# Performance work log

Hardware: AMD Instinct MI355X
Metric: run time of the kernel (lower is better)

The kernel has to match this reference:

```python
import jax, jax.numpy as jnp
import numpy as np

N, E, H, C, L, D, OUT = 50000, 800000, 4, 32, 3, 128, 64
EPS = 1e-5


def setup_inputs() -> dict:
    key = jax.random.key(0)
    ks = jax.random.split(key, 16)
    s = 1.0 / np.sqrt(D)
    return {
        "x": jax.random.normal(ks[0], (N, D), jnp.float32),
        "edge_index": jax.random.randint(ks[1], (2, E), 0, N, dtype=jnp.int32),
        "Wq": jax.random.normal(ks[2], (L, D, H * C), jnp.float32) * s,
        "bq": jax.random.normal(ks[3], (L, H * C), jnp.float32) * 0.02,
        "Wk": jax.random.normal(ks[4], (L, D, H * C), jnp.float32) * s,
        "bk": jax.random.normal(ks[5], (L, H * C), jnp.float32) * 0.02,
        "Wv": jax.random.normal(ks[6], (L, D, H * C), jnp.float32) * s,
        "bv": jax.random.normal(ks[7], (L, H * C), jnp.float32) * 0.02,
        "Ws": jax.random.normal(ks[8], (L, D, H * C), jnp.float32) * s,
        "bs": jax.random.normal(ks[9], (L, H * C), jnp.float32) * 0.02,
        "bn_g": jnp.ones((L, H * C), jnp.float32),
        "bn_b": jnp.zeros((L, H * C), jnp.float32),
        "W_out": jax.random.normal(ks[10], (D, OUT), jnp.float32) * s,
        "b_out": jax.random.normal(ks[11], (OUT,), jnp.float32) * 0.02,
        "bno_g": jnp.ones((OUT,), jnp.float32),
        "bno_b": jnp.zeros((OUT,), jnp.float32),
    }


def _batch_norm(x, g, b):
    # training-mode BatchNorm1d: per-feature batch mean/var (biased), eps=1e-5
    mu = x.mean(axis=0)
    var = x.var(axis=0)
    return g * (x - mu) * jax.lax.rsqrt(var + EPS) + b


def _transformer_conv(x, src, dst, Wq, bq, Wk, bk, Wv, bv, Ws, bs):
    n = x.shape[0]
    q = (x @ Wq + bq).reshape(n, H, C)  # query at target nodes
    k = (x @ Wk + bk).reshape(n, H, C)
    v = (x @ Wv + bv).reshape(n, H, C)
    # per-edge attention logits [E, H]
    score = (q[dst] * k[src]).sum(-1) / jnp.sqrt(jnp.float32(C))
    # numerically-stable softmax over incoming edges of each target node
    m = jax.ops.segment_max(score, dst, num_segments=n)
    ex = jnp.exp(score - m[dst])
    denom = jax.ops.segment_sum(ex, dst, num_segments=n)
    alpha = ex / denom[dst]  # [E, H]
    agg = jax.ops.segment_sum(v[src] * alpha[..., None], dst, num_segments=n)
    out = agg.reshape(n, H * C) + x @ Ws + bs  # concat heads + root/skip term
    return out


def reference(x, edge_index, Wq, bq, Wk, bk, Wv, bv, Ws, bs, bn_g, bn_b,
              W_out, b_out, bno_g, bno_b):
    src, dst = edge_index[0], edge_index[1]
    h = x
    for i in range(L):
        h = _transformer_conv(h, src, dst, Wq[i], bq[i], Wk[i], bk[i],
                              Wv[i], bv[i], Ws[i], bs[i])
        h = _batch_norm(h, bn_g[i], bn_b[i])
        h = jax.nn.relu(h)
    h = h @ W_out + b_out
    h = _batch_norm(h, bno_g, bno_b)
    return jax.nn.relu(h)
```

## Files before the change

### kernel.cpp

```cpp
#include <hip/hip_runtime.h>
#include <hip/hip_bf16.h>
#include <math.h>

#define D_FEAT 128
#define NLAYER 3
#define BN_EPS 1e-5f
#define INV_SQRT_C 0.17677669529663687f
#define SORT_NPB 1024
#define NREP 8

typedef __bf16 bf16x8 __attribute__((ext_vector_type(8)));
typedef float f32x4 __attribute__((ext_vector_type(4)));

static __device__ __forceinline__ unsigned short f2bf(float f) {
    return __builtin_bit_cast(unsigned short, __float2bfloat16(f));
}
static __device__ __forceinline__ float bfl(unsigned u) { return __uint_as_float(u << 16); }
static __device__ __forceinline__ float bfh(unsigned u) { return __uint_as_float(u & 0xffff0000u); }
static __device__ __forceinline__ unsigned packbf(float a, float b) {
    return (unsigned)f2bf(a) | ((unsigned)f2bf(b) << 16);
}


__global__ void cvt_bf16_kernel(const float* __restrict__ src, unsigned short* __restrict__ dst,
                                size_t n4) {
    for (size_t t = (size_t)blockIdx.x * blockDim.x + threadIdx.x; t < n4;
         t += (size_t)gridDim.x * blockDim.x) {
        size_t i = t * 4;
        float4 v = *(const float4*)(src + i);
        ushort4 u;
        u.x = f2bf(v.x); u.y = f2bf(v.y); u.z = f2bf(v.z); u.w = f2bf(v.w);
        *(ushort4*)(dst + i) = u;
    }
}

__global__ void prep_weights_kernel(
    const float* __restrict__ Wq, const float* __restrict__ Wk,
    const float* __restrict__ Wv, const float* __restrict__ Ws,
    const float* __restrict__ Wo,
    unsigned short* __restrict__ Wt, unsigned short* __restrict__ Wot)
{
    const int permat = 16384;
    const int main_total = NLAYER * 4 * permat;
    const int total = main_total + 64 * 128;
    for (int i = blockIdx.x * blockDim.x + threadIdx.x; i < total;
         i += gridDim.x * blockDim.x) {
        if (i < main_total) {
            int l = i / (4 * permat);
            int rem = i - l * (4 * permat);
            int mat = rem / permat;
            int e = rem - mat * permat;
            int nn = e >> 7;
            int kk = e & 127;
            const float* src = (mat == 0) ? Wq : (mat == 1) ? Wk : (mat == 2) ? Wv : Ws;
            Wt[(size_t)l * 4 * permat + mat * permat + nn * 128 + kk] =
                f2bf(src[(size_t)l * permat + kk * 128 + nn]);
        } else {
            int e = i - main_total;
            int nn = e >> 7;
            int kk = e & 127;
            Wot[nn * 128 + kk] = f2bf(Wo[kk * 64 + nn]);
        }
    }
}


__global__ void hist_kernel(const int* __restrict__ dst, int E, int* __restrict__ deg) {
    int e = blockIdx.x * blockDim.x + threadIdx.x;
    if (e < E) atomicAdd(&deg[dst[e]], 1);
}

__global__ __launch_bounds__(256) void scan1_kernel(const int* __restrict__ deg, int n,
                                                    int* __restrict__ rowptr,
                                                    int* __restrict__ partials) {
    int b = blockIdx.x, tid = threadIdx.x;
    int base = b * 1024 + tid * 4;
    int4 d = {0, 0, 0, 0};
    if (base + 3 < n) d = *(const int4*)(deg + base);
    else {
        if (base + 0 < n) d.x = deg[base + 0];
        if (base + 1 < n) d.y = deg[base + 1];
        if (base + 2 < n) d.z = deg[base + 2];
        if (base + 3 < n) d.w = deg[base + 3];
    }
    int p0 = d.x, p1 = p0 + d.y, p2 = p1 + d.z, p3 = p2 + d.w;
    int v = p3;
    int lane = tid & 63;
    #pragma unroll
    for (int off = 1; off < 64; off <<= 1) {
        int t = __shfl_up(v, off);
        if (lane >= off) v += t;
    }
    __shared__ int wsum[4];
    int w = tid >> 6;
    if (lane == 63) wsum[w] = v;
    __syncthreads();
    int woff = 0;
    #pragma unroll
    for (int j = 0; j < 4; ++j) if (j < w) woff += wsum[j];
    int excl = woff + v - p3;
    if (base + 0 < n) rowptr[base + 1] = excl + p0;
    if (base + 1 < n) rowptr[base + 2] = excl + p1;
    if (base + 2 < n) rowptr[base + 3] = excl + p2;
    if (base + 3 < n) rowptr[base + 4] = excl + p3;
    if (tid == 255) partials[b] = excl + p3;
    if (b == 0 && tid == 0) rowptr[0] = 0;
}

__global__ void scan2_kernel(int* __restrict__ partials, int nb) {
    int lane = threadIdx.x;
    int v = (lane < nb) ? partials[lane] : 0;
    #pragma unroll
    for (int off = 1; off < 64; off <<= 1) {
        int t = __shfl_up(v, off);
        if (lane >= off) v += t;
    }
    if (lane < nb) partials[lane] = v;
}

__global__ __launch_bounds__(256) void scan3_kernel(int* __restrict__ rowptr, int n,
                                                    const int* __restrict__ partials) {
    int b = blockIdx.x, tid = threadIdx.x;
    if (b == 0) return;
    int off = partials[b - 1];
    int base = b * 1024 + tid * 4;
    #pragma unroll
    for (int j = 0; j < 4; ++j) {
        int i = base + j;
        if (i < n) rowptr[i + 1] += off;
    }
}

__global__ void scatter_kernel(const int* __restrict__ src, const int* __restrict__ dst, int E,
                               const int* __restrict__ rowptr, int* __restrict__ cursor,
                               int* __restrict__ csrsrc) {
    int e = blockIdx.x * blockDim.x + threadIdx.x;
    if (e < E) {
        int d = dst[e];
        int p = atomicAdd(&cursor[d], 1);
        csrsrc[rowptr[d] + p] = src[e];
    }
}


__global__ __launch_bounds__(256) void bin_blockhist_kernel(
    const int* __restrict__ rowptr, int n, int B, int* __restrict__ bhist)
{
    __shared__ int h[256];
    int b = blockIdx.x, tid = threadIdx.x;
    h[tid] = 0;
    __syncthreads();
    #pragma unroll
    for (int j = 0; j < SORT_NPB / 256; ++j) {
        int i = b * SORT_NPB + j * 256 + tid;
        if (i < n) {
            int d = rowptr[i + 1] - rowptr[i];
            if (d > 255) d = 255;
            atomicAdd(&h[255 - d], 1);
        }
    }
    __syncthreads();
    bhist[tid * B + b] = h[tid];
}

__global__ __launch_bounds__(256) void bin_colscan_kernel(
    int* __restrict__ bhist, int B, int* __restrict__ binoff)
{
    int d = threadIdx.x;
    int run = 0;
    for (int b = 0; b < B; ++b) {
        int c = bhist[d * B + b];
        bhist[d * B + b] = run;
        run += c;
    }
    __shared__ int sd[256];
    sd[d] = run;
    __syncthreads();
    int v = run;
    for (int s = 1; s < 256; s <<= 1) {
        int t = (d >= s) ? sd[d - s] : 0;
        __syncthreads();
        sd[d] += t;
        __syncthreads();
    }
    binoff[d] = sd[d] - v;
}

__global__ __launch_bounds__(256) void bin_order_kernel(
    const int* __restrict__ rowptr, int n, int B,
    const int* __restrict__ bhist, const int* __restrict__ binoff,
    int* __restrict__ order)
{
    __shared__ int cur[256];
    int b = blockIdx.x, tid = threadIdx.x;
    cur[tid] = binoff[tid] + bhist[tid * B + b];
    __syncthreads();
    #pragma unroll
    for (int j = 0; j < SORT_NPB / 256; ++j) {
        int i = b * SORT_NPB + j * 256 + tid;
        if (i < n) {
            int d = rowptr[i + 1] - rowptr[i];
            if (d > 255) d = 255;
            int pos = atomicAdd(&cur[255 - d], 1);
            order[pos] = i;
        }
    }
}


__global__ __launch_bounds__(256, 2) void gemm_qkvs_kernel(
    const unsigned short* __restrict__ A,
    const float* __restrict__ stats, const float* __restrict__ g,
    const float* __restrict__ bb, int mode, int M,
    const unsigned short* __restrict__ Wt,
    const float* __restrict__ b0, const float* __restrict__ b1,
    const float* __restrict__ b2, const float* __restrict__ b3,
    unsigned short* __restrict__ q, unsigned short* __restrict__ kv,
    unsigned short* __restrict__ s)
{
    __shared__ float scale[128], shift[128];
    int r0 = blockIdx.x * 128;
    int tid = threadIdx.x;
    int wid = tid >> 6, lane = tid & 63;
    int wm = wid >> 1, wn = wid & 1;
    int lr = lane & 15, lk = lane >> 4;

    if (mode && tid < 128) {
        float ssum = 0.f, qsum = 0.f;
        #pragma unroll
        for (int r = 0; r < NREP; ++r) {
            ssum += stats[r * 1024 + tid];
            qsum += stats[r * 1024 + 512 + tid];
        }
        float invN = 1.0f / (float)M;
        float mu = ssum * invN;
        float var = qsum * invN - mu * mu;
        float sc = rsqrtf(var + BN_EPS) * g[tid];
        scale[tid] = sc;
        shift[tid] = bb[tid] - mu * sc;
    }
    __syncthreads();

    bf16x8 a[4][4];
    #pragma unroll
    for (int ks = 0; ks < 4; ++ks) {
        int ko = ks * 32 + lk * 8;
        #pragma unroll
        for (int mi = 0; mi < 4; ++mi) {
            int arow = r0 + wm * 64 + mi * 16 + lr;
            int4 t = {0, 0, 0, 0};
            if (arow < M) t = *(const int4*)(A + (size_t)arow * 128 + ko);
            if (mode) {
                float4 sc0 = *(const float4*)&scale[ko];
                float4 sc1 = *(const float4*)&scale[ko + 4];
                float4 sh0 = *(const float4*)&shift[ko];
                float4 sh1 = *(const float4*)&shift[ko + 4];
                float v0 = fmaxf(bfl(t.x) * sc0.x + sh0.x, 0.f);
                float v1 = fmaxf(bfh(t.x) * sc0.y + sh0.y, 0.f);
                float v2 = fmaxf(bfl(t.y) * sc0.z + sh0.z, 0.f);
                float v3 = fmaxf(bfh(t.y) * sc0.w + sh0.w, 0.f);
                float v4 = fmaxf(bfl(t.z) * sc1.x + sh1.x, 0.f);
                float v5 = fmaxf(bfh(t.z) * sc1.y + sh1.y, 0.f);
                float v6 = fmaxf(bfl(t.w) * sc1.z + sh1.z, 0.f);
                float v7 = fmaxf(bfh(t.w) * sc1.w + sh1.w, 0.f);
                t.x = (int)packbf(v0, v1); t.y = (int)packbf(v2, v3);
                t.z = (int)packbf(v4, v5); t.w = (int)packbf(v6, v7);
            }
            a[mi][ks] = __builtin_bit_cast(bf16x8, t);
        }
    }

    #pragma unroll
    for (int cc = 0; cc < 2; ++cc) {
        int ct = blockIdx.y * 2 + cc;
        const unsigned short* W = Wt + (size_t)ct * 16384;

        f32x4 acc[4][4] = {};
        #pragma unroll
        for (int ks = 0; ks < 4; ++ks) {
            int ko = ks * 32 + lk * 8;
            bf16x8 b[4];
            #pragma unroll
            for (int nj = 0; nj < 4; ++nj) {
                int4 t = *(const int4*)(W + (size_t)(wn * 64 + nj * 16 + lr) * 128 + ko);
                b[nj] = __builtin_bit_cast(bf16x8, t);
            }
            #pragma unroll
            for (int mi = 0; mi < 4; ++mi)
                #pragma unroll
                for (int nj = 0; nj < 4; ++nj)
                    acc[mi][nj] = __builtin_amdgcn_mfma_f32_16x16x32_bf16(
                        a[mi][ks], b[nj], acc[mi][nj], 0, 0, 0);
        }

        const float* bias = (ct == 0) ? b0 : (ct == 1) ? b1 : (ct == 2) ? b2 : b3;
        #pragma unroll
        for (int mi = 0; mi < 4; ++mi) {
            #pragma unroll
            for (int nj = 0; nj < 4; ++nj) {
                int col = wn * 64 + nj * 16 + lr;
                float bv = bias[col];
                #pragma unroll
                for (int reg = 0; reg < 4; ++reg) {
                    int rw = r0 + wm * 64 + mi * 16 + lk * 4 + reg;
                    if (rw < M) {
                        unsigned short val = f2bf(acc[mi][nj][reg] + bv);
                        if (ct == 0) q[(size_t)rw * 128 + col] = val;
                        else if (ct == 1) kv[(size_t)rw * 256 + col] = val;
                        else if (ct == 2) kv[(size_t)rw * 256 + 128 + col] = val;
                        else s[(size_t)rw * 128 + col] = val;
                    }
                }
            }
        }
    }
}

__global__ __launch_bounds__(256, 2) void gemm_final_kernel(
    const unsigned short* __restrict__ A,
    const float* __restrict__ stats, const float* __restrict__ g,
    const float* __restrict__ bb, int M,
    const unsigned short* __restrict__ Wot, const float* __restrict__ bias,
    float* __restrict__ out, float* __restrict__ statsOut)
{
    __shared__ float scale[128], shift[128];
    __shared__ float fs[64], fq[64];
    int r0 = blockIdx.x * 128;
    int tid = threadIdx.x;
    int wid = tid >> 6, lane = tid & 63;
    int wm = wid >> 1, wn = wid & 1;
    int lr = lane & 15, lk = lane >> 4;

    if (tid < 128) {
        float ssum = 0.f, qsum = 0.f;
        #pragma unroll
        for (int r = 0; r < NREP; ++r) {
            ssum += stats[r * 1024 + tid];
            qsum += stats[r * 1024 + 512 + tid];
        }
        float invN = 1.0f / (float)M;
        float mu = ssum * invN;
        float var = qsum * invN - mu * mu;
        float sc = rsqrtf(var + BN_EPS) * g[tid];
        scale[tid] = sc;
        shift[tid] = bb[tid] - mu * sc;
    }
    if (tid < 64) { fs[tid] = 0.f; fq[tid] = 0.f; }
    __syncthreads();

    bf16x8 a[4][4];
    #pragma unroll
    for (int ks = 0; ks < 4; ++ks) {
        int ko = ks * 32 + lk * 8;
        #pragma unroll
        for (int mi = 0; mi < 4; ++mi) {
            int arow = r0 + wm * 64 + mi * 16 + lr;
            int4 t = {0, 0, 0, 0};
            if (arow < M) t = *(const int4*)(A + (size_t)arow * 128 + ko);
            float4 sc0 = *(const float4*)&scale[ko];
            float4 sc1 = *(const float4*)&scale[ko + 4];
            float4 sh0 = *(const float4*)&shift[ko];
            float4 sh1 = *(const float4*)&shift[ko + 4];
            float v0 = fmaxf(bfl(t.x) * sc0.x + sh0.x, 0.f);
            float v1 = fmaxf(bfh(t.x) * sc0.y + sh0.y, 0.f);
            float v2 = fmaxf(bfl(t.y) * sc0.z + sh0.z, 0.f);
            float v3 = fmaxf(bfh(t.y) * sc0.w + sh0.w, 0.f);
            float v4 = fmaxf(bfl(t.z) * sc1.x + sh1.x, 0.f);
            float v5 = fmaxf(bfh(t.z) * sc1.y + sh1.y, 0.f);
            float v6 = fmaxf(bfl(t.w) * sc1.z + sh1.z, 0.f);
            float v7 = fmaxf(bfh(t.w) * sc1.w + sh1.w, 0.f);
            t.x = (int)packbf(v0, v1); t.y = (int)packbf(v2, v3);
            t.z = (int)packbf(v4, v5); t.w = (int)packbf(v6, v7);
            a[mi][ks] = __builtin_bit_cast(bf16x8, t);
        }
    }

    f32x4 acc[4][2] = {};
    #pragma unroll
    for (int ks = 0; ks < 4; ++ks) {
        int ko = ks * 32 + lk * 8;
        bf16x8 b[2];
        #pragma unroll
        for (int nj = 0; nj < 2; ++nj) {
            int4 t = *(const int4*)(Wot + (size_t)(wn * 32 + nj * 16 + lr) * 128 + ko);
            b[nj] = __builtin_bit_cast(bf16x8, t);
        }
        #pragma unroll
        for (int mi = 0; mi < 4; ++mi)
            #pragma unroll
            for (int nj = 0; nj < 2; ++nj)
                acc[mi][nj] = __builtin_amdgcn_mfma_f32_16x16x32_bf16(
                    a[mi][ks], b[nj], acc[mi][nj], 0, 0, 0);
    }

    float csum[2] = {0.f, 0.f}, csq[2] = {0.f, 0.f};
    #pragma unroll
    for (int mi = 0; mi < 4; ++mi) {
        #pragma unroll
        for (int nj = 0; nj < 2; ++nj) {
            int col = wn * 32 + nj * 16 + lr;
            float bv = bias[col];
            #pragma unroll
            for (int reg = 0; reg < 4; ++reg) {
                int rw = r0 + wm * 64 + mi * 16 + lk * 4 + reg;
                if (rw < M) {
                    float val = acc[mi][nj][reg] + bv;
                    out[(size_t)rw * 64 + col] = val;
                    csum[nj] += val;
                    csq[nj] += val * val;
                }
            }
        }
    }
    #pragma unroll
    for (int nj = 0; nj < 2; ++nj) {
        csum[nj] += __shfl_xor(csum[nj], 16);
        csum[nj] += __shfl_xor(csum[nj], 32);
        csq[nj]  += __shfl_xor(csq[nj], 16);
        csq[nj]  += __shfl_xor(csq[nj], 32);
    }
    if (lane < 16) {
        #pragma unroll
        for (int nj = 0; nj < 2; ++nj) {
            int col = wn * 32 + nj * 16 + lr;
            atomicAdd(&fs[col], csum[nj]);
            atomicAdd(&fq[col], csq[nj]);
        }
    }
    __syncthreads();
    if (tid < 64) atomicAdd(&statsOut[tid], fs[tid]);
    else if (tid < 128) atomicAdd(&statsOut[512 + tid - 64], fq[tid - 64]);
}


__global__ __launch_bounds__(256) void attn_kernel(
    const unsigned short* __restrict__ q, const unsigned short* __restrict__ kv,
    const unsigned short* __restrict__ sk,
    const int* __restrict__ rowptr, const int* __restrict__ csrsrc,
    const int* __restrict__ order,
    unsigned short* __restrict__ hnext, float* __restrict__ stats, int N)
{
    __shared__ float ls[128], lq2[128];
    int tid = threadIdx.x;
    if (tid < 128) { ls[tid] = 0.f; lq2[tid] = 0.f; }
    __syncthreads();

    int wave = (blockIdx.x * blockDim.x + tid) >> 6;
    int lane = tid & 63;
    int gl = lane & 15;
    int slot = wave * 4 + (lane >> 4);
    bool nv = slot < N;
    int n = nv ? order[slot] : 0;

    int r0 = rowptr[n], r1 = rowptr[n + 1];
    int deg = nv ? (r1 - r0) : 0;
    int dmax = deg;
    dmax = max(dmax, __shfl_xor(dmax, 16));
    dmax = max(dmax, __shfl_xor(dmax, 32));

    int4 qu = *(const int4*)(q + (size_t)n * 128 + gl * 8);
    float qf[8];
    qf[0] = bfl(qu.x); qf[1] = bfh(qu.x); qf[2] = bfl(qu.y); qf[3] = bfh(qu.y);
    qf[4] = bfl(qu.z); qf[5] = bfh(qu.z); qf[6] = bfl(qu.w); qf[7] = bfh(qu.w);

    float m = -INFINITY, ssum = 0.f;
    float acc[8] = {};

    for (int i = 0; i < dmax; i += 8) {
        int eidx[8];
        bool av[8];
        #pragma unroll
        for (int j = 0; j < 8; ++j) {
            av[j] = (i + j) < deg;
            int e = csrsrc[r0 + i + j];
            eidx[j] = av[j] ? e : 0;
        }
        int4 K[8], V[8];
        #pragma unroll
        for (int j = 0; j < 8; ++j) {
            const unsigned short* row = kv + (size_t)eidx[j] * 256 + gl * 8;
            K[j] = *(const int4*)(row);
            V[j] = *(const int4*)(row + 128);
        }
        float sc[8];
        #pragma unroll
        for (int j = 0; j < 8; ++j) {
            float p = qf[0] * bfl(K[j].x) + qf[1] * bfh(K[j].x)
                    + qf[2] * bfl(K[j].y) + qf[3] * bfh(K[j].y)
                    + qf[4] * bfl(K[j].z) + qf[5] * bfh(K[j].z)
                    + qf[6] * bfl(K[j].w) + qf[7] * bfh(K[j].w);
            p += __shfl_xor(p, 1);
            p += __shfl_xor(p, 2);
            sc[j] = av[j] ? p * INV_SQRT_C : -INFINITY;
        }
        float mn = m;
        #pragma unroll
        for (int j = 0; j < 8; ++j) mn = fmaxf(mn, sc[j]);
        if (mn > m) {
            float scale = __expf(m - mn);
            ssum *= scale;
            #pragma unroll
            for (int c = 0; c < 8; ++c) acc[c] *= scale;
            m = mn;
        }
        #pragma unroll
        for (int j = 0; j < 8; ++j) {
            float ej = av[j] ? __expf(sc[j] - m) : 0.f;
            ssum += ej;
            acc[0] += ej * bfl(V[j].x); acc[1] += ej * bfh(V[j].x);
            acc[2] += ej * bfl(V[j].y); acc[3] += ej * bfh(V[j].y);
            acc[4] += ej * bfl(V[j].z); acc[5] += ej * bfh(V[j].z);
            acc[6] += ej * bfl(V[j].w); acc[7] += ej * bfh(V[j].w);
        }
    }

    float o[8];
    if (nv) {
        float inv = (ssum > 0.f) ? 1.0f / ssum : 0.f;
        int4 su = *(const int4*)(sk + (size_t)n * 128 + gl * 8);
        o[0] = acc[0] * inv + bfl(su.x); o[1] = acc[1] * inv + bfh(su.x);
        o[2] = acc[2] * inv + bfl(su.y); o[3] = acc[3] * inv + bfh(su.y);
        o[4] = acc[4] * inv + bfl(su.z); o[5] = acc[5] * inv + bfh(su.z);
        o[6] = acc[6] * inv + bfl(su.w); o[7] = acc[7] * inv + bfh(su.w);
        int4 st;
        st.x = (int)packbf(o[0], o[1]); st.y = (int)packbf(o[2], o[3]);
        st.z = (int)packbf(o[4], o[5]); st.w = (int)packbf(o[6], o[7]);
        *(int4*)(hnext + (size_t)n * 128 + gl * 8) = st;
    } else {
        #pragma unroll
        for (int c = 0; c < 8; ++c) o[c] = 0.f;
    }

    float s8[8], q8[8];
    #pragma unroll
    for (int c = 0; c < 8; ++c) { s8[c] = o[c]; q8[c] = o[c] * o[c]; }
    #pragma unroll
    for (int c = 0; c < 8; ++c) {
        s8[c] += __shfl_xor(s8[c], 16); s8[c] += __shfl_xor(s8[c], 32);
        q8[c] += __shfl_xor(q8[c], 16); q8[c] += __shfl_xor(q8[c], 32);
    }
    if (lane < 16) {
        #pragma unroll
        for (int c = 0; c < 8; ++c) {
            atomicAdd(&ls[gl * 8 + c], s8[c]);
            atomicAdd(&lq2[gl * 8 + c], q8[c]);
        }
    }
    __syncthreads();
    float* srep = stats + (blockIdx.x & (NREP - 1)) * 1024;
    if (tid < 128) atomicAdd(&srep[tid], ls[tid]);
    else atomicAdd(&srep[512 + tid - 128], lq2[tid - 128]);
}


__global__ __launch_bounds__(256) void bn_apply_f32_kernel(
    const float* __restrict__ x, float* __restrict__ y,
    const float* __restrict__ stats, const float* __restrict__ g,
    const float* __restrict__ b, int N, int F)
{
    __shared__ float scale[128], shift[128];
    int tid = threadIdx.x;
    if (tid < F) {
        float invN = 1.0f / (float)N;
        float mu = stats[tid] * invN;
        float var = stats[512 + tid] * invN - mu * mu;
        float sc = rsqrtf(var + BN_EPS) * g[tid];
        scale[tid] = sc;
        shift[tid] = b[tid] - mu * sc;
    }
    __syncthreads();
    size_t total4 = (size_t)N * F >> 2;
    int Fm = F - 1;
    for (size_t t = (size_t)blockIdx.x * blockDim.x + tid; t < total4;
         t += (size_t)gridDim.x * blockDim.x) {
        size_t i = t * 4;
        int f = (int)(i & (size_t)Fm);
        float4 v = *(const float4*)(x + i);
        float4 o;
        o.x = fmaxf(v.x * scale[f + 0] + shift[f + 0], 0.f);
        o.y = fmaxf(v.y * scale[f + 1] + shift[f + 1], 0.f);
        o.z = fmaxf(v.z * scale[f + 2] + shift[f + 2], 0.f);
        o.w = fmaxf(v.w * scale[f + 3] + shift[f + 3], 0.f);
        *(float4*)(y + i) = o;
    }
}


static inline size_t al16(size_t x) { return (x + 15) & ~(size_t)15; }

extern "C" void kernel_launch(void* const* d_in, const int* in_sizes, int n_in,
                              void* d_out, int out_size, void* d_ws, size_t ws_size,
                              hipStream_t stream) {
    const float* x    = (const float*)d_in[0];
    const int*   edge = (const int*)d_in[1];
    const float* Wq   = (const float*)d_in[2];
    const float* bq   = (const float*)d_in[3];
    const float* Wk   = (const float*)d_in[4];
    const float* bk   = (const float*)d_in[5];
    const float* Wv   = (const float*)d_in[6];
    const float* bv   = (const float*)d_in[7];
    const float* Wsk  = (const float*)d_in[8];
    const float* bsk  = (const float*)d_in[9];
    const float* bng  = (const float*)d_in[10];
    const float* bnb  = (const float*)d_in[11];
    const float* Wo   = (const float*)d_in[12];
    const float* bo   = (const float*)d_in[13];
    const float* bnog = (const float*)d_in[14];
    const float* bnob = (const float*)d_in[15];

    const int N = in_sizes[0] / D_FEAT;
    const int E = in_sizes[1] / 2;
    const int* esrc = edge;
    const int* edst = edge + E;

    const int SB = (N + SORT_NPB - 1) / SORT_NPB;

    char* wsb = (char*)d_ws;
    unsigned short* xb = (unsigned short*)wsb; wsb += al16((size_t)N * 128 * 2);
    unsigned short* kv = (unsigned short*)wsb; wsb += al16((size_t)N * 256 * 2);
    unsigned short* q  = (unsigned short*)wsb; wsb += al16((size_t)N * 128 * 2);
    unsigned short* s  = (unsigned short*)wsb; wsb += al16((size_t)N * 128 * 2);
    unsigned short* hnext = (unsigned short*)wsb; wsb += al16((size_t)N * 128 * 2);
    float* outpre = (float*)wsb; wsb += al16((size_t)N * 64 * 4);
    unsigned short* Wt  = (unsigned short*)wsb; wsb += al16((size_t)NLAYER * 4 * 16384 * 2);
    unsigned short* Wot = (unsigned short*)wsb; wsb += al16((size_t)64 * 128 * 2);
    float* stats  = (float*)wsb; wsb += al16((size_t)(NLAYER * NREP + 1) * 1024 * 4);
    int* rowptr   = (int*)wsb;   wsb += al16((size_t)(N + 1) * 4);
    int* deg      = (int*)wsb;   wsb += al16((size_t)N * 4);
    int* csrsrc   = (int*)wsb;   wsb += al16((size_t)(E + 64) * 4);
    int* partials = (int*)wsb;   wsb += al16(256 * 4);
    int* bhist    = (int*)wsb;   wsb += al16((size_t)256 * SB * 4);
    int* binoff   = (int*)wsb;   wsb += al16(256 * 4);
    int* order    = (int*)wsb;   wsb += al16((size_t)N * 4);

    cvt_bf16_kernel<<<2048, 256, 0, stream>>>(x, xb, (size_t)N * 128 / 4);
    prep_weights_kernel<<<256, 256, 0, stream>>>(Wq, Wk, Wv, Wsk, Wo, Wt, Wot);
    hipMemsetAsync(stats, 0, (size_t)(NLAYER * NREP + 1) * 1024 * 4, stream);

    const int nb1 = (N + 1023) / 1024;
    hipMemsetAsync(deg, 0, (size_t)N * 4, stream);
    hist_kernel<<<(E + 255) / 256, 256, 0, stream>>>(edst, E, deg);
    scan1_kernel<<<nb1, 256, 0, stream>>>(deg, N, rowptr, partials);
    scan2_kernel<<<1, 64, 0, stream>>>(partials, nb1);
    scan3_kernel<<<nb1, 256, 0, stream>>>(rowptr, N, partials);
    hipMemsetAsync(deg, 0, (size_t)N * 4, stream);
    scatter_kernel<<<(E + 255) / 256, 256, 0, stream>>>(esrc, edst, E, rowptr, deg, csrsrc);

    bin_blockhist_kernel<<<SB, 256, 0, stream>>>(rowptr, N, SB, bhist);
    bin_colscan_kernel<<<1, 256, 0, stream>>>(bhist, SB, binoff);
    bin_order_kernel<<<SB, 256, 0, stream>>>(rowptr, N, SB, bhist, binoff, order);

    const int gemm_rb = (N + 127) / 128;
    const int attn_blocks = (N + 15) / 16;
    const unsigned short* hin = xb;
    for (int l = 0; l < NLAYER; ++l) {
        const float* statsIn = (l == 0) ? (const float*)nullptr
                                        : stats + (size_t)(l - 1) * NREP * 1024;
        const float* gIn = (l == 0) ? (const float*)nullptr : bng + (l - 1) * 128;
        const float* bIn = (l == 0) ? (const float*)nullptr : bnb + (l - 1) * 128;
        gemm_qkvs_kernel<<<dim3(gemm_rb, 2), 256, 0, stream>>>(
            hin, statsIn, gIn, bIn, (l == 0) ? 0 : 1, N,
            Wt + (size_t)l * 4 * 16384,
            bq + l * 128, bk + l * 128, bv + l * 128, bsk + l * 128,
            q, kv, s);
        attn_kernel<<<attn_blocks, 256, 0, stream>>>(q, kv, s, rowptr, csrsrc, order,
                                                     hnext, stats + (size_t)l * NREP * 1024, N);
        hin = hnext;
    }

    float* fstats = stats + (size_t)NLAYER * NREP * 1024;
    gemm_final_kernel<<<gemm_rb, 256, 0, stream>>>(
        hnext, stats + (size_t)2 * NREP * 1024, bng + 2 * 128, bnb + 2 * 128, N,
        Wot, bo, outpre, fstats);
    bn_apply_f32_kernel<<<2048, 256, 0, stream>>>(outpre, (float*)d_out, fstats,
                                                  bnog, bnob, N, 64);
}
```

Baseline: 491.5 us.

## Fuse prep and CSR-build launches, coalesce GEMM epilogue stores via LDS

Merges input conversion and weight transposition into one kernel, collapses three memsets into one by placing the zeroed buffers next to each other, and fuses the scan fix-up with the degree-bin histogram. The QKVS GEMM epilogue now stages bf16 results in a padded shared tile and writes 16-byte coalesced rows instead of scattered 2-byte stores. This cuts launch overhead and uncoalesced writes, at the cost of extra LDS and two block barriers per column tile.

```diff
diff --git a/kernel.cpp b/kernel.cpp
--- a/kernel.cpp
+++ b/kernel.cpp
@@ -8,6 +8,7 @@
 #define INV_SQRT_C 0.17677669529663687f
 #define SORT_NPB 1024
 #define NREP 8
+#define TP 136
 
 typedef __bf16 bf16x8 __attribute__((ext_vector_type(8)));
 typedef float f32x4 __attribute__((ext_vector_type(4)));
@@ -22,44 +23,47 @@
 }
 
 
-__global__ void cvt_bf16_kernel(const float* __restrict__ src, unsigned short* __restrict__ dst,
-                                size_t n4) {
-    for (size_t t = (size_t)blockIdx.x * blockDim.x + threadIdx.x; t < n4;
-         t += (size_t)gridDim.x * blockDim.x) {
-        size_t i = t * 4;
-        float4 v = *(const float4*)(src + i);
-        ushort4 u;
-        u.x = f2bf(v.x); u.y = f2bf(v.y); u.z = f2bf(v.z); u.w = f2bf(v.w);
-        *(ushort4*)(dst + i) = u;
-    }
-}
-
-__global__ void prep_weights_kernel(
-    const float* __restrict__ Wq, const float* __restrict__ Wk,
-    const float* __restrict__ Wv, const float* __restrict__ Ws,
-    const float* __restrict__ Wo,
-    unsigned short* __restrict__ Wt, unsigned short* __restrict__ Wot)
-{
-    const int permat = 16384;
-    const int main_total = NLAYER * 4 * permat;
-    const int total = main_total + 64 * 128;
-    for (int i = blockIdx.x * blockDim.x + threadIdx.x; i < total;
-         i += gridDim.x * blockDim.x) {
-        if (i < main_total) {
-            int l = i / (4 * permat);
-            int rem = i - l * (4 * permat);
-            int mat = rem / permat;
-            int e = rem - mat * permat;
-            int nn = e >> 7;
-            int kk = e & 127;
-            const float* src = (mat == 0) ? Wq : (mat == 1) ? Wk : (mat == 2) ? Wv : Ws;
-            Wt[(size_t)l * 4 * permat + mat * permat + nn * 128 + kk] =
-                f2bf(src[(size_t)l * permat + kk * 128 + nn]);
-        } else {
-            int e = i - main_total;
-            int nn = e >> 7;
-            int kk = e & 127;
-            Wot[nn * 128 + kk] = f2bf(Wo[kk * 64 + nn]);
+__global__ void prep_kernel(const float* __restrict__ x, unsigned short* __restrict__ xb,
+                            size_t n4,
+                            const float* __restrict__ Wq, const float* __restrict__ Wk,
+                            const float* __restrict__ Wv, const float* __restrict__ Ws,
+                            const float* __restrict__ Wo,
+                            unsigned short* __restrict__ Wt, unsigned short* __restrict__ Wot)
+{
+    const int CVTB = 1792;
+    int b = blockIdx.x;
+    if (b < CVTB) {
+        for (size_t t = (size_t)b * blockDim.x + threadIdx.x; t < n4;
+             t += (size_t)CVTB * blockDim.x) {
+            size_t i = t * 4;
+            float4 v = *(const float4*)(x + i);
+            ushort4 u;
+            u.x = f2bf(v.x); u.y = f2bf(v.y); u.z = f2bf(v.z); u.w = f2bf(v.w);
+            *(ushort4*)(xb + i) = u;
+        }
+    } else {
+        const int permat = 16384;
+        const int main_total = NLAYER * 4 * permat;
+        const int total = main_total + 64 * 128;
+        const int WB = gridDim.x - CVTB;
+        for (int i = (b - CVTB) * blockDim.x + threadIdx.x; i < total;
+             i += WB * blockDim.x) {
+            if (i < main_total) {
+                int l = i / (4 * permat);
+                int rem = i - l * (4 * permat);
+                int mat = rem / permat;
+                int e = rem - mat * permat;
+                int nn = e >> 7;
+                int kk = e & 127;
+                const float* src = (mat == 0) ? Wq : (mat == 1) ? Wk : (mat == 2) ? Wv : Ws;
+                Wt[(size_t)l * 4 * permat + mat * permat + nn * 128 + kk] =
+                    f2bf(src[(size_t)l * permat + kk * 128 + nn]);
+            } else {
+                int e = i - main_total;
+                int nn = e >> 7;
+                int kk = e & 127;
+                Wot[nn * 128 + kk] = f2bf(Wo[kk * 64 + nn]);
+            }
         }
     }
 }
@@ -118,17 +122,35 @@
     if (lane < nb) partials[lane] = v;
 }
 
-__global__ __launch_bounds__(256) void scan3_kernel(int* __restrict__ rowptr, int n,
-                                                    const int* __restrict__ partials) {
+__global__ __launch_bounds__(256) void scan3_hist_kernel(
+    int* __restrict__ rowptr, int n, const int* __restrict__ partials,
+    int B, int* __restrict__ bhist)
+{
+    __shared__ int h[256];
+    __shared__ int oldv[SORT_NPB];
     int b = blockIdx.x, tid = threadIdx.x;
-    if (b == 0) return;
-    int off = partials[b - 1];
-    int base = b * 1024 + tid * 4;
-    #pragma unroll
-    for (int j = 0; j < 4; ++j) {
-        int i = base + j;
-        if (i < n) rowptr[i + 1] += off;
-    }
+    h[tid] = 0;
+    int off = (b == 0) ? 0 : partials[b - 1];
+    #pragma unroll
+    for (int j = 0; j < SORT_NPB / 256; ++j) {
+        int loc = j * 256 + tid;
+        int i = b * SORT_NPB + loc;
+        oldv[loc] = (i < n) ? rowptr[i + 1] : 0;
+    }
+    __syncthreads();
+    #pragma unroll
+    for (int j = 0; j < SORT_NPB / 256; ++j) {
+        int loc = j * 256 + tid;
+        int i = b * SORT_NPB + loc;
+        if (i < n) {
+            int d = (loc == 0) ? oldv[0] : (oldv[loc] - oldv[loc - 1]);
+            if (d > 255) d = 255;
+            atomicAdd(&h[255 - d], 1);
+            rowptr[i + 1] = oldv[loc] + off;
+        }
+    }
+    __syncthreads();
+    bhist[tid * B + b] = h[tid];
 }
 
 __global__ void scatter_kernel(const int* __restrict__ src, const int* __restrict__ dst, int E,
@@ -140,27 +162,6 @@
         int p = atomicAdd(&cursor[d], 1);
         csrsrc[rowptr[d] + p] = src[e];
     }
-}
-
-
-__global__ __launch_bounds__(256) void bin_blockhist_kernel(
-    const int* __restrict__ rowptr, int n, int B, int* __restrict__ bhist)
-{
-    __shared__ int h[256];
-    int b = blockIdx.x, tid = threadIdx.x;
-    h[tid] = 0;
-    __syncthreads();
-    #pragma unroll
-    for (int j = 0; j < SORT_NPB / 256; ++j) {
-        int i = b * SORT_NPB + j * 256 + tid;
-        if (i < n) {
-            int d = rowptr[i + 1] - rowptr[i];
-            if (d > 255) d = 255;
-            atomicAdd(&h[255 - d], 1);
-        }
-    }
-    __syncthreads();
-    bhist[tid * B + b] = h[tid];
 }
 
 __global__ __launch_bounds__(256) void bin_colscan_kernel(
@@ -219,6 +220,7 @@
     unsigned short* __restrict__ s)
 {
     __shared__ float scale[128], shift[128];
+    __shared__ unsigned short tile[128 * TP];
     int r0 = blockIdx.x * 128;
     int tid = threadIdx.x;
     int wid = tid >> 6, lane = tid & 63;
@@ -294,6 +296,7 @@
         }
 
         const float* bias = (ct == 0) ? b0 : (ct == 1) ? b1 : (ct == 2) ? b2 : b3;
+        __syncthreads();
         #pragma unroll
         for (int mi = 0; mi < 4; ++mi) {
             #pragma unroll
@@ -302,15 +305,23 @@
                 float bv = bias[col];
                 #pragma unroll
                 for (int reg = 0; reg < 4; ++reg) {
-                    int rw = r0 + wm * 64 + mi * 16 + lk * 4 + reg;
-                    if (rw < M) {
-                        unsigned short val = f2bf(acc[mi][nj][reg] + bv);
-                        if (ct == 0) q[(size_t)rw * 128 + col] = val;
-                        else if (ct == 1) kv[(size_t)rw * 256 + col] = val;
-                        else if (ct == 2) kv[(size_t)rw * 256 + 128 + col] = val;
-                        else s[(size_t)rw * 128 + col] = val;
-                    }
+                    int rloc = wm * 64 + mi * 16 + lk * 4 + reg;
+                    tile[rloc * TP + col] = f2bf(acc[mi][nj][reg] + bv);
                 }
+            }
+        }
+        __syncthreads();
+        #pragma unroll
+        for (int it = 0; it < 8; ++it) {
+            int flat = (it * 256 + tid) * 8;
+            int row = flat >> 7, col = flat & 127;
+            int rw = r0 + row;
+            if (rw < M) {
+                int4 v = *(const int4*)&tile[row * TP + col];
+                if (ct == 0) *(int4*)(q + (size_t)rw * 128 + col) = v;
+                else if (ct == 1) *(int4*)(kv + (size_t)rw * 256 + col) = v;
+                else if (ct == 2) *(int4*)(kv + (size_t)rw * 256 + 128 + col) = v;
+                else *(int4*)(s + (size_t)rw * 128 + col) = v;
             }
         }
     }
@@ -614,6 +625,7 @@
     const int* edst = edge + E;
 
     const int SB = (N + SORT_NPB - 1) / SORT_NPB;
+    const size_t STATS_F = (size_t)(NLAYER * NREP + 1) * 1024;
 
     char* wsb = (char*)d_ws;
     unsigned short* xb = (unsigned short*)wsb; wsb += al16((size_t)N * 128 * 2);
@@ -624,29 +636,27 @@
     float* outpre = (float*)wsb; wsb += al16((size_t)N * 64 * 4);
     unsigned short* Wt  = (unsigned short*)wsb; wsb += al16((size_t)NLAYER * 4 * 16384 * 2);
     unsigned short* Wot = (unsigned short*)wsb; wsb += al16((size_t)64 * 128 * 2);
-    float* stats  = (float*)wsb; wsb += al16((size_t)(NLAYER * NREP + 1) * 1024 * 4);
+    float* stats  = (float*)wsb; wsb += al16(STATS_F * 4);
+    int* deg      = (int*)wsb;   wsb += al16((size_t)N * 4);
+    int* cursor   = (int*)wsb;   wsb += al16((size_t)N * 4);
+    size_t zero_bytes = (char*)wsb - (char*)stats;
     int* rowptr   = (int*)wsb;   wsb += al16((size_t)(N + 1) * 4);
-    int* deg      = (int*)wsb;   wsb += al16((size_t)N * 4);
     int* csrsrc   = (int*)wsb;   wsb += al16((size_t)(E + 64) * 4);
     int* partials = (int*)wsb;   wsb += al16(256 * 4);
     int* bhist    = (int*)wsb;   wsb += al16((size_t)256 * SB * 4);
     int* binoff   = (int*)wsb;   wsb += al16(256 * 4);
     int* order    = (int*)wsb;   wsb += al16((size_t)N * 4);
 
-    cvt_bf16_kernel<<<2048, 256, 0, stream>>>(x, xb, (size_t)N * 128 / 4);
-    prep_weights_kernel<<<256, 256, 0, stream>>>(Wq, Wk, Wv, Wsk, Wo, Wt, Wot);
-    hipMemsetAsync(stats, 0, (size_t)(NLAYER * NREP + 1) * 1024 * 4, stream);
+    prep_kernel<<<2048, 256, 0, stream>>>(x, xb, (size_t)N * 128 / 4,
+                                          Wq, Wk, Wv, Wsk, Wo, Wt, Wot);
+    hipMemsetAsync(stats, 0, zero_bytes, stream);
 
     const int nb1 = (N + 1023) / 1024;
-    hipMemsetAsync(deg, 0, (size_t)N * 4, stream);
     hist_kernel<<<(E + 255) / 256, 256, 0, stream>>>(edst, E, deg);
     scan1_kernel<<<nb1, 256, 0, stream>>>(deg, N, rowptr, partials);
     scan2_kernel<<<1, 64, 0, stream>>>(partials, nb1);
-    scan3_kernel<<<nb1, 256, 0, stream>>>(rowptr, N, partials);
-    hipMemsetAsync(deg, 0, (size_t)N * 4, stream);
-    scatter_kernel<<<(E + 255) / 256, 256, 0, stream>>>(esrc, edst, E, rowptr, deg, csrsrc);
-
-    bin_blockhist_kernel<<<SB, 256, 0, stream>>>(rowptr, N, SB, bhist);
+    scan3_hist_kernel<<<SB, 256, 0, stream>>>(rowptr, N, partials, SB, bhist);
+    scatter_kernel<<<(E + 255) / 256, 256, 0, stream>>>(esrc, edst, E, rowptr, cursor, csrsrc);
     bin_colscan_kernel<<<1, 256, 0, stream>>>(bhist, SB, binoff);
     bin_order_kernel<<<SB, 256, 0, stream>>>(rowptr, N, SB, bhist, binoff, order);
 
```

Result: faster. 446.8 us (-9.1%).
